# Kernel optimization log

Measured on AMD Instinct MI355X. Metric: run time of the kernel, lower is better.

The kernel has to match this reference:

```python
import jax, jax.numpy as jnp
import numpy as np
import math

B, S, D, H = 4, 2048, 1024, 16
HD = D // H  # head_dim = 64


def setup_inputs() -> dict:
    key = jax.random.key(0)
    ks = jax.random.split(key, 12)
    inv = 1.0 / math.sqrt(D)
    inp = {
        "query": jax.random.normal(ks[0], (B, S, D), dtype=jnp.float32),
        "key": jax.random.normal(ks[1], (B, S, D), dtype=jnp.float32),
        "value": jax.random.normal(ks[2], (B, S, D), dtype=jnp.float32),
        # causal mask, broadcast over heads; guarantees no all-masked softmax rows
        "mask": jnp.tril(jnp.ones((S, S), dtype=jnp.int32))[None, None].repeat(B, axis=0),
        # linear params stored as (in, out); y = x @ W + b (same math as torch Linear)
        "Wq": jax.random.uniform(ks[3], (D, D), jnp.float32, -inv, inv),
        "bq": jax.random.uniform(ks[4], (D,), jnp.float32, -inv, inv),
        "Wk": jax.random.uniform(ks[5], (D, D), jnp.float32, -inv, inv),
        "bk": jax.random.uniform(ks[6], (D,), jnp.float32, -inv, inv),
        "Wv": jax.random.uniform(ks[7], (D, D), jnp.float32, -inv, inv),
        "bv": jax.random.uniform(ks[8], (D,), jnp.float32, -inv, inv),
        "Wo": jax.random.uniform(ks[9], (D, D), jnp.float32, -inv, inv),
        "bo": jax.random.uniform(ks[10], (D,), jnp.float32, -inv, inv),
    }
    return inp


def _split_heads(x):
    # [B, S, D] -> [B, H, S, HD]
    b, s, _ = x.shape
    return x.reshape(b, s, H, HD).transpose(0, 2, 1, 3)


def reference(query, key, value, mask, Wq, bq, Wk, bk, Wv, bv, Wo, bo):
    q = _split_heads(query @ Wq + bq)   # [B,H,S,HD]
    k = _split_heads(key @ Wk + bk)
    v = _split_heads(value @ Wv + bv)
    scores = jnp.einsum("bhqd,bhkd->bhqk", q, k)          # [B,H,S,S]
    scores = jnp.where(mask == 0, -jnp.inf, scores)
    attn = jax.nn.softmax(scores / math.sqrt(HD), axis=-1)
    attn = attn * mask.astype(attn.dtype)                  # post-softmax re-mask (as in source)
    out = jnp.einsum("bhqk,bhkd->bhqd", attn, v)           # [B,H,S,HD]
    out = out.transpose(0, 2, 1, 3).reshape(query.shape[0], -1, D)
    return out @ Wo + bo
```

## Files before the change

### kernel.cpp

```cpp
#include <hip/hip_runtime.h>

typedef __attribute__((ext_vector_type(8))) short short8;
typedef __attribute__((ext_vector_type(8))) unsigned short ushort8;
typedef __attribute__((ext_vector_type(4))) unsigned short us4;
typedef __attribute__((ext_vector_type(4))) float f32x4;
typedef __attribute__((ext_vector_type(4))) int i32x4;

#define S_LEN 2048
#define D_MODEL 1024
#define N_HEADS 16
#define HEAD_DIM 64

__device__ __forceinline__ unsigned short f2bf(float f) {
  union { float f; unsigned u; } x; x.f = f;
  unsigned r = x.u + 0x7FFFu + ((x.u >> 16) & 1u);
  return (unsigned short)(r >> 16);
}

__device__ __forceinline__ int pkbf(float a, float b) {
  union { float f; unsigned u; } x, y;
  x.f = a; y.f = b;
  return (int)__builtin_amdgcn_perm(y.u + 0x8000u, x.u + 0x8000u, 0x07060302u);
}

__global__ __launch_bounds__(256) void cvt3_kernel(const float* __restrict__ a,
                                                   const float* __restrict__ b,
                                                   const float* __restrict__ c,
                                                   unsigned short* __restrict__ oa,
                                                   unsigned short* __restrict__ ob,
                                                   unsigned short* __restrict__ oc) {
  int bid = blockIdx.x;
  const float* in = (bid < 4096) ? a : (bid < 8192 ? b : c);
  unsigned short* out = (bid < 4096) ? oa : (bid < 8192 ? ob : oc);
  int i = (bid & 4095) * 256 + threadIdx.x;
  const f32x4* in4 = (const f32x4*)in;
  f32x4 x = in4[2 * i], y = in4[2 * i + 1];
  i32x4 o;
  o[0] = pkbf(x[0], x[1]);
  o[1] = pkbf(x[2], x[3]);
  o[2] = pkbf(y[0], y[1]);
  o[3] = pkbf(y[2], y[3]);
  ((i32x4*)out)[i] = o;
}

__global__ __launch_bounds__(256) void transpose_w4(
    const float* __restrict__ Wq, const float* __restrict__ Wk,
    const float* __restrict__ Wv, const float* __restrict__ Wo,
    unsigned short* __restrict__ wqkvT, unsigned short* __restrict__ woT) {
  __shared__ float tile[64][65];
  const int z = blockIdx.z;
  const float* W = (z == 0) ? Wq : (z == 1) ? Wk : (z == 2) ? Wv : Wo;
  unsigned short* Wt = (z < 3) ? (wqkvT + (size_t)z * D_MODEL * D_MODEL) : woT;
  const int no = blockIdx.x * 64, ko = blockIdx.y * 64;
  const int tx = threadIdx.x & 63, ty = threadIdx.x >> 6;
  for (int r = ty; r < 64; r += 4)
    tile[r][tx] = W[(size_t)(ko + r) * D_MODEL + no + tx];
  __syncthreads();
  for (int r = ty; r < 64; r += 4)
    Wt[(size_t)(no + r) * D_MODEL + ko + tx] = f2bf(tile[tx][r]);
}

template <int MODE>
__global__ __launch_bounds__(512) void proj_gemm(
    const unsigned short* __restrict__ A0,
    const unsigned short* __restrict__ A1,
    const unsigned short* __restrict__ A2,
    const unsigned short* __restrict__ Bt,
    const float* __restrict__ b0p, const float* __restrict__ b1p,
    const float* __restrict__ b2p,
    void* __restrict__ o0, void* __restrict__ o1, void* __restrict__ o2,
    float qscale) {
  extern __shared__ __align__(16) unsigned short smem_d[];
  const int tid = threadIdx.x;
  const int wave = tid >> 6, lane = tid & 63;
  const int quad = lane >> 4, l16 = lane & 15;

  const int nlin = blockIdx.y * (MODE == 0 ? 24 : 8) + blockIdx.x;
  const int xcd = nlin & 7;
  const int j = nlin >> 3;
  int bx_eff, by_eff;
  if (MODE == 0) {
    by_eff = xcd * 4 + ((j >> 3) & 3);
    bx_eff = (j >> 5) * 8 + (j & 7);
  } else {
    by_eff = xcd * 4 + (j >> 3);
    bx_eff = j & 7;
  }
  const int m0 = by_eff * 256, n0 = bx_eff * 128;
  const int wm = (wave >> 1) * 64, wn = (wave & 1) * 64;

  const int sel = (MODE == 0) ? (n0 >> 10) : 0;
  const unsigned short* A = (MODE == 0) ? (sel == 0 ? A0 : sel == 1 ? A1 : A2) : A0;
  const float* bias = (MODE == 0) ? (sel == 0 ? b0p : sel == 1 ? b1p : b2p) : b0p;
  const float scale = (MODE == 0 && sel == 0) ? qscale : 1.0f;
  const int nb = (MODE == 0) ? (n0 & 1023) : n0;

  f32x4 acc[4][4] = {};

  const int srw = wave * 8 + (lane >> 3);
  const int sch = ((lane & 7) ^ ((lane >> 3) & 7)) << 3;

  auto stage = [&](int kt, int half) {
    unsigned short* Ab = smem_d + (kt % 3) * 24576;
    unsigned short* Bb = Ab + 16384;
    const int k0 = kt * 64;
#pragma unroll
    for (int rr = 0; rr < 2; ++rr) {
      const int rd = half * 2 + rr;
      const unsigned short* g = A + (size_t)(m0 + rd * 64 + srw) * D_MODEL + k0 + sch;
      __builtin_amdgcn_global_load_lds((const __attribute__((address_space(1))) void*)g,
          (__attribute__((address_space(3))) void*)(Ab + rd * 4096 + wave * 512), 16, 0, 0);
    }
    const unsigned short* gb = Bt + (size_t)(n0 + half * 64 + srw) * D_MODEL + k0 + sch;
    __builtin_amdgcn_global_load_lds((const __attribute__((address_space(1))) void*)gb,
        (__attribute__((address_space(3))) void*)(Bb + half * 4096 + wave * 512), 16, 0, 0);
  };

  stage(0, 0); stage(0, 1); stage(1, 0); stage(1, 1);
  asm volatile("s_waitcnt vmcnt(6)" ::: "memory");
  __builtin_amdgcn_s_barrier();

  for (int kt = 0; kt < 16; ++kt) {
    const unsigned short* Ab = smem_d + (kt % 3) * 24576;
    const unsigned short* Bb = Ab + 16384;
#pragma unroll
    for (int t = 0; t < 2; ++t) {
      if (kt + 2 < 16) stage(kt + 2, t);
      short8 af[4], bf[4];
#pragma unroll
      for (int i = 0; i < 4; ++i) {
        int r = wm + i * 16 + l16;
        af[i] = *(const short8*)(Ab + r * 64 + (((t * 4 + quad) ^ (r & 7)) << 3));
      }
#pragma unroll
      for (int j2 = 0; j2 < 4; ++j2) {
        int r = wn + j2 * 16 + l16;
        bf[j2] = *(const short8*)(Bb + r * 64 + (((t * 4 + quad) ^ (r & 7)) << 3));
      }
      __builtin_amdgcn_s_barrier();
      __builtin_amdgcn_s_setprio(1);
#pragma unroll
      for (int i = 0; i < 4; ++i)
#pragma unroll
        for (int j2 = 0; j2 < 4; ++j2)
          acc[i][j2] = __builtin_amdgcn_mfma_f32_16x16x32_bf16(af[i], bf[j2], acc[i][j2], 0, 0, 0);
      __builtin_amdgcn_s_setprio(0);
      __builtin_amdgcn_s_barrier();
    }
    if (kt + 2 < 16) {
      asm volatile("s_waitcnt vmcnt(6)" ::: "memory");
    } else {
      asm volatile("s_waitcnt vmcnt(0)" ::: "memory");
    }
  }

  float bv4[4];
#pragma unroll
  for (int j2 = 0; j2 < 4; ++j2) bv4[j2] = bias[nb + wn + j2 * 16 + l16];

  if (MODE == 0) {
    if (sel < 2) {
      unsigned short* T = smem_d + wave * 1152;
      unsigned short* out = (unsigned short*)(sel == 0 ? o0 : o1);
      const int h = (nb + wn) >> 6;
#pragma unroll
      for (int i = 0; i < 4; ++i) {
#pragma unroll
        for (int j2 = 0; j2 < 4; ++j2)
#pragma unroll
          for (int r = 0; r < 4; ++r)
            T[(quad * 4 + r) * 72 + j2 * 16 + l16] = f2bf((acc[i][j2][r] + bv4[j2]) * scale);
        int m = m0 + wm + i * 16 + l16;
        int b = m >> 11, s = m & 2047;
#pragma unroll
        for (int t = 0; t < 2; ++t) {
          short8 row = *(const short8*)(T + l16 * 72 + t * 32 + quad * 8);
          *(short8*)(out + (((size_t)(b * N_HEADS + h) * S_LEN + s) << 6) + t * 32 + quad * 8) = row;
        }
      }
    } else {
      unsigned short* vt = (unsigned short*)o2;
#pragma unroll
      for (int i = 0; i < 4; ++i) {
        int m = m0 + wm + i * 16 + quad * 4;
        int b = m >> 11, s = m & 2047;
#pragma unroll
        for (int j2 = 0; j2 < 4; ++j2) {
          int n = nb + wn + j2 * 16 + l16;
          int h = n >> 6, d = n & 63;
          us4 pv;
#pragma unroll
          for (int r = 0; r < 4; ++r) pv[r] = f2bf(acc[i][j2][r] + bv4[j2]);
          *(us4*)(vt + (((size_t)(b * N_HEADS + h) * 64 + d) << 11) + s) = pv;
        }
      }
    }
  } else {
    float* Tf = (float*)smem_d + wave * 1088;
    float* out = (float*)o0;
#pragma unroll
    for (int i = 0; i < 4; ++i) {
#pragma unroll
      for (int j2 = 0; j2 < 4; ++j2)
#pragma unroll
        for (int r = 0; r < 4; ++r)
          Tf[(quad * 4 + r) * 68 + j2 * 16 + l16] = acc[i][j2][r] + bv4[j2];
      int m = m0 + wm + i * 16 + l16;
#pragma unroll
      for (int t = 0; t < 4; ++t) {
        f32x4 row = *(const f32x4*)(Tf + l16 * 68 + t * 16 + quad * 4);
        *(f32x4*)(out + (size_t)m * D_MODEL + nb + wn + t * 16 + quad * 4) = row;
      }
    }
  }
}

__global__ __launch_bounds__(256, 4) void flash_attn(
    const unsigned short* __restrict__ Qh,
    const unsigned short* __restrict__ Kh,
    const unsigned short* __restrict__ Vt,
    unsigned short* __restrict__ ctx) {
  __shared__ __align__(16) unsigned short smem[16384];
  const int tid = threadIdx.x;
  const int wave = tid >> 6, lane = tid & 63;
  const int quad = lane >> 4, l16 = lane & 15;
  const int l7 = l16 & 7;

  const int nlin = blockIdx.y * 16 + blockIdx.x;
  const int xcd = nlin & 7;
  const int rr = nlin >> 3;
  const int bh = xcd * 8 + (rr & 7);
  const int qslot = rr >> 3;
  const int qa = qslot & 3, qb = qslot >> 2;
  const int qbase = qa + ((qb >> 1) << 2);
  const int qi = (qb & 1) ? (15 - qbase) : qbase;
  const int q0 = qi * 128;
  const int nk = 2 * qi + 2;
  const size_t hb = (size_t)bh * (S_LEN * HEAD_DIM);
  const int srow = lane >> 3;
  const int schunk = ((lane & 7) ^ srow) * 8;

  auto stage = [&](int kt, int buf) {
    unsigned short* Kb = smem + buf * 8192;
    unsigned short* Vb = smem + buf * 8192 + 4096;
#pragma unroll
    for (int c = 0; c < 2; ++c) {
      int row = wave * 16 + c * 8 + srow;
      const unsigned short* gk = Kh + hb + (size_t)(kt * 64 + row) * 64 + schunk;
      __builtin_amdgcn_global_load_lds((const __attribute__((address_space(1))) void*)gk,
          (__attribute__((address_space(3))) void*)(Kb + (wave * 16 + c * 8) * 64), 16, 0, 0);
      const unsigned short* gv = Vt + hb + (size_t)row * S_LEN + kt * 64 + schunk;
      __builtin_amdgcn_global_load_lds((const __attribute__((address_space(1))) void*)gv,
          (__attribute__((address_space(3))) void*)(Vb + (wave * 16 + c * 8) * 64), 16, 0, 0);
    }
  };

  stage(0, 0);

  short8 qf[2][2];
#pragma unroll
  for (int s = 0; s < 2; ++s)
#pragma unroll
    for (int t = 0; t < 2; ++t)
      qf[s][t] = *(const short8*)(Qh + hb +
          (size_t)(q0 + wave * 32 + s * 16 + l16) * 64 + t * 32 + quad * 8);

  f32x4 o[4][2] = {};
  float rsum[2] = {0.f, 0.f};

  for (int kt = 0; kt < nk; ++kt) {
    __syncthreads();
    if (kt + 1 < nk) stage(kt + 1, (kt + 1) & 1);
    const unsigned short* Kb = smem + (kt & 1) * 8192;
    const unsigned short* Vb = Kb + 4096;

    if (kt * 64 > q0 + wave * 32 + 31) continue;

    f32x4 sc[2][4];
    __builtin_amdgcn_s_setprio(1);
#pragma unroll
    for (int nt = 0; nt < 4; ++nt) {
      short8 k0 = *(const short8*)(Kb + (nt * 16 + l16) * 64 + ((quad ^ l7) << 3));
      short8 k1 = *(const short8*)(Kb + (nt * 16 + l16) * 64 + (((4 + quad) ^ l7) << 3));
#pragma unroll
      for (int s = 0; s < 2; ++s) {
        f32x4 z = {};
        z = __builtin_amdgcn_mfma_f32_16x16x32_bf16(k0, qf[s][0], z, 0, 0, 0);
        sc[s][nt] = __builtin_amdgcn_mfma_f32_16x16x32_bf16(k1, qf[s][1], z, 0, 0, 0);
      }
    }
    __builtin_amdgcn_s_setprio(0);
    if (kt >= 2 * qi) {
#pragma unroll
      for (int s = 0; s < 2; ++s) {
        int qg = q0 + wave * 32 + s * 16 + l16;
#pragma unroll
        for (int nt = 0; nt < 4; ++nt) {
          int kg = kt * 64 + nt * 16 + quad * 4;
#pragma unroll
          for (int r = 0; r < 4; ++r)
            if (kg + r > qg) sc[s][nt][r] = -1e30f;
        }
      }
    }

    union { int i[4]; short8 v; } pf[2][2];
#pragma unroll
    for (int s = 0; s < 2; ++s) {
      int pk[4][2];
#pragma unroll
      for (int nt = 0; nt < 4; ++nt) {
        float p0 = __builtin_amdgcn_exp2f(sc[s][nt][0]);
        float p1 = __builtin_amdgcn_exp2f(sc[s][nt][1]);
        float p2 = __builtin_amdgcn_exp2f(sc[s][nt][2]);
        float p3 = __builtin_amdgcn_exp2f(sc[s][nt][3]);
        rsum[s] += (p0 + p1) + (p2 + p3);
        pk[nt][0] = pkbf(p0, p1);
        pk[nt][1] = pkbf(p2, p3);
      }
#pragma unroll
      for (int t = 0; t < 2; ++t) {
        int A = pk[t * 2][0], C = pk[t * 2 + 1][0];
        int B2 = pk[t * 2][1], D = pk[t * 2 + 1][1];
        asm("v_permlane32_swap_b32 %0, %1" : "+v"(A), "+v"(C));
        asm("v_permlane16_swap_b32 %0, %1" : "+v"(A), "+v"(C));
        asm("v_permlane32_swap_b32 %0, %1" : "+v"(B2), "+v"(D));
        asm("v_permlane16_swap_b32 %0, %1" : "+v"(B2), "+v"(D));
        pf[s][t].i[0] = A;
        pf[s][t].i[1] = B2;
        pf[s][t].i[2] = C;
        pf[s][t].i[3] = D;
      }
    }

    __builtin_amdgcn_s_setprio(1);
#pragma unroll
    for (int ntd = 0; ntd < 4; ++ntd) {
      short8 v0 = *(const short8*)(Vb + (ntd * 16 + l16) * 64 + ((quad ^ l7) << 3));
      short8 v1 = *(const short8*)(Vb + (ntd * 16 + l16) * 64 + (((4 + quad) ^ l7) << 3));
#pragma unroll
      for (int s = 0; s < 2; ++s) {
        o[ntd][s] = __builtin_amdgcn_mfma_f32_16x16x32_bf16(v0, pf[s][0].v, o[ntd][s], 0, 0, 0);
        o[ntd][s] = __builtin_amdgcn_mfma_f32_16x16x32_bf16(v1, pf[s][1].v, o[ntd][s], 0, 0, 0);
      }
    }
    __builtin_amdgcn_s_setprio(0);
  }

#pragma unroll
  for (int s = 0; s < 2; ++s) {
    rsum[s] += __shfl_xor(rsum[s], 16, 64);
    rsum[s] += __shfl_xor(rsum[s], 32, 64);
  }

  __syncthreads();
  unsigned short* Os = smem;
#pragma unroll
  for (int s = 0; s < 2; ++s) {
    float invl = 1.0f / rsum[s];
#pragma unroll
    for (int ntd = 0; ntd < 4; ++ntd) {
      us4 pk4;
#pragma unroll
      for (int r = 0; r < 4; ++r) pk4[r] = f2bf(o[ntd][s][r] * invl);
      *(us4*)(Os + (wave * 32 + s * 16 + l16) * 72 + ntd * 16 + quad * 4) = pk4;
    }
  }
  __syncthreads();
  const int b = bh >> 4, h = bh & 15;
#pragma unroll
  for (int it = 0; it < 4; ++it) {
    int e = it * 256 + tid;
    int row = e >> 3, c = (e & 7) * 8;
    short8 vrow = *(const short8*)(Os + row * 72 + c);
    *(short8*)(ctx + (size_t)(b * S_LEN + q0 + row) * D_MODEL + h * HEAD_DIM + c) = vrow;
  }
}

extern "C" void kernel_launch(void* const* d_in, const int* in_sizes, int n_in,
                              void* d_out, int out_size, void* d_ws, size_t ws_size,
                              hipStream_t stream) {
  (void)in_sizes; (void)n_in; (void)out_size;
  const float* q  = (const float*)d_in[0];
  const float* k  = (const float*)d_in[1];
  const float* v  = (const float*)d_in[2];
  const float* Wq = (const float*)d_in[4];
  const float* bq = (const float*)d_in[5];
  const float* Wk = (const float*)d_in[6];
  const float* bk = (const float*)d_in[7];
  const float* Wv = (const float*)d_in[8];
  const float* bv = (const float*)d_in[9];
  const float* Wo = (const float*)d_in[10];
  const float* bo = (const float*)d_in[11];
  float* out = (float*)d_out;

  if (ws_size < 109051904u) return;
  char* ws = (char*)d_ws;
  unsigned short* xq    = (unsigned short*)(ws);
  unsigned short* xk    = (unsigned short*)(ws + 16777216);
  unsigned short* xv    = (unsigned short*)(ws + 33554432);
  unsigned short* wqkvT = (unsigned short*)(ws + 50331648);
  unsigned short* woT   = (unsigned short*)(ws + 56623104);
  unsigned short* qh    = (unsigned short*)(ws + 58720256);
  unsigned short* kh    = qh + 8388608;
  unsigned short* vt    = kh + 8388608;
  unsigned short* ctx   = xq;

  static int attr_done = 0;
  if (!attr_done) {
    auto* k0f = proj_gemm<0>;
    auto* k1f = proj_gemm<1>;
    hipFuncSetAttribute(reinterpret_cast<const void*>(k0f),
                        hipFuncAttributeMaxDynamicSharedMemorySize, 147456);
    hipFuncSetAttribute(reinterpret_cast<const void*>(k1f),
                        hipFuncAttributeMaxDynamicSharedMemorySize, 147456);
    attr_done = 1;
  }

  cvt3_kernel<<<12288, 256, 0, stream>>>(q, k, v, xq, xk, xv);
  transpose_w4<<<dim3(16, 16, 4), 256, 0, stream>>>(Wq, Wk, Wv, Wo, wqkvT, woT);
  proj_gemm<0><<<dim3(24, 32), 512, 147456, stream>>>(xq, xk, xv, wqkvT, bq, bk, bv,
                                                      qh, kh, vt, 0.125f * 1.44269504088896f);
  flash_attn<<<dim3(16, 64), 256, 0, stream>>>(qh, kh, vt, ctx);
  proj_gemm<1><<<dim3(8, 32), 512, 147456, stream>>>(ctx, ctx, ctx, woT, bo, bo, bo,
                                                     out, out, out, 1.0f);
}
```

Baseline: 322.2 us.

## Shrink projection GEMM tiles to 128x128 with 256 threads and deeper K pipeline

Reworks the projection GEMM from 256x128 tiles with 512 threads and a K-step of 64 to 128x128 tiles with 256 threads, a K-step of 32 and a three-deep prefetch. LDS use drops from 144KB to 48KB, so up to three blocks can share a CU, and the grid doubles to spread work across more CUs. The block-to-XCD mapping and the LDS swizzle are remapped to match. The trade-off is less operand reuse per tile, more barriers per K iteration, and more global traffic for A and B.

```diff
diff --git a/kernel.cpp b/kernel.cpp
--- a/kernel.cpp
+++ b/kernel.cpp
@@ -61,7 +61,7 @@
 }
 
 template <int MODE>
-__global__ __launch_bounds__(512) void proj_gemm(
+__global__ __launch_bounds__(256, 3) void proj_gemm(
     const unsigned short* __restrict__ A0,
     const unsigned short* __restrict__ A1,
     const unsigned short* __restrict__ A2,
@@ -80,13 +80,15 @@
   const int j = nlin >> 3;
   int bx_eff, by_eff;
   if (MODE == 0) {
-    by_eff = xcd * 4 + ((j >> 3) & 3);
-    bx_eff = (j >> 5) * 8 + (j & 7);
+    const int sel_i = j >> 6;
+    const int rem = j & 63;
+    by_eff = xcd * 8 + (rem >> 3);
+    bx_eff = sel_i * 8 + (rem & 7);
   } else {
-    by_eff = xcd * 4 + (j >> 3);
+    by_eff = xcd * 8 + (j >> 3);
     bx_eff = j & 7;
   }
-  const int m0 = by_eff * 256, n0 = bx_eff * 128;
+  const int m0 = by_eff * 128, n0 = bx_eff * 128;
   const int wm = (wave >> 1) * 64, wn = (wave & 1) * 64;
 
   const int sel = (MODE == 0) ? (n0 >> 10) : 0;
@@ -97,61 +99,62 @@
 
   f32x4 acc[4][4] = {};
 
-  const int srw = wave * 8 + (lane >> 3);
-  const int sch = ((lane & 7) ^ ((lane >> 3) & 7)) << 3;
-
-  auto stage = [&](int kt, int half) {
-    unsigned short* Ab = smem_d + (kt % 3) * 24576;
-    unsigned short* Bb = Ab + 16384;
-    const int k0 = kt * 64;
-#pragma unroll
-    for (int rr = 0; rr < 2; ++rr) {
-      const int rd = half * 2 + rr;
-      const unsigned short* g = A + (size_t)(m0 + rd * 64 + srw) * D_MODEL + k0 + sch;
-      __builtin_amdgcn_global_load_lds((const __attribute__((address_space(1))) void*)g,
-          (__attribute__((address_space(3))) void*)(Ab + rd * 4096 + wave * 512), 16, 0, 0);
-    }
-    const unsigned short* gb = Bt + (size_t)(n0 + half * 64 + srw) * D_MODEL + k0 + sch;
-    __builtin_amdgcn_global_load_lds((const __attribute__((address_space(1))) void*)gb,
-        (__attribute__((address_space(3))) void*)(Bb + half * 4096 + wave * 512), 16, 0, 0);
+  const int lrow = lane >> 2;
+  const int kcs = ((lane & 3) ^ (lrow & 3)) << 3;
+
+  auto stage = [&](int kt) {
+    unsigned short* Ab = smem_d + (kt % 3) * 8192;
+    unsigned short* Bb = Ab + 4096;
+    const int k0 = kt * 32;
+#pragma unroll
+    for (int c = 0; c < 2; ++c) {
+      const int r = wave * 32 + c * 16;
+      const unsigned short* ga = A + (size_t)(m0 + r + lrow) * D_MODEL + k0 + kcs;
+      __builtin_amdgcn_global_load_lds((const __attribute__((address_space(1))) void*)ga,
+          (__attribute__((address_space(3))) void*)(Ab + r * 32), 16, 0, 0);
+      const unsigned short* gb = Bt + (size_t)(n0 + r + lrow) * D_MODEL + k0 + kcs;
+      __builtin_amdgcn_global_load_lds((const __attribute__((address_space(1))) void*)gb,
+          (__attribute__((address_space(3))) void*)(Bb + r * 32), 16, 0, 0);
+    }
   };
 
-  stage(0, 0); stage(0, 1); stage(1, 0); stage(1, 1);
-  asm volatile("s_waitcnt vmcnt(6)" ::: "memory");
+  const int fsw = (quad ^ (l16 & 3)) << 3;
+
+  stage(0); stage(1); stage(2);
+  asm volatile("s_waitcnt vmcnt(8)" ::: "memory");
   __builtin_amdgcn_s_barrier();
-
-  for (int kt = 0; kt < 16; ++kt) {
-    const unsigned short* Ab = smem_d + (kt % 3) * 24576;
-    const unsigned short* Bb = Ab + 16384;
-#pragma unroll
-    for (int t = 0; t < 2; ++t) {
-      if (kt + 2 < 16) stage(kt + 2, t);
-      short8 af[4], bf[4];
-#pragma unroll
-      for (int i = 0; i < 4; ++i) {
-        int r = wm + i * 16 + l16;
-        af[i] = *(const short8*)(Ab + r * 64 + (((t * 4 + quad) ^ (r & 7)) << 3));
-      }
-#pragma unroll
-      for (int j2 = 0; j2 < 4; ++j2) {
-        int r = wn + j2 * 16 + l16;
-        bf[j2] = *(const short8*)(Bb + r * 64 + (((t * 4 + quad) ^ (r & 7)) << 3));
-      }
-      __builtin_amdgcn_s_barrier();
-      __builtin_amdgcn_s_setprio(1);
-#pragma unroll
-      for (int i = 0; i < 4; ++i)
-#pragma unroll
-        for (int j2 = 0; j2 < 4; ++j2)
-          acc[i][j2] = __builtin_amdgcn_mfma_f32_16x16x32_bf16(af[i], bf[j2], acc[i][j2], 0, 0, 0);
-      __builtin_amdgcn_s_setprio(0);
-      __builtin_amdgcn_s_barrier();
-    }
-    if (kt + 2 < 16) {
-      asm volatile("s_waitcnt vmcnt(6)" ::: "memory");
-    } else {
+  __builtin_amdgcn_sched_barrier(0);
+
+  for (int kt = 0; kt < 32; ++kt) {
+    const unsigned short* Ab = smem_d + (kt % 3) * 8192;
+    const unsigned short* Bb = Ab + 4096;
+    short8 af[4], bf[4];
+#pragma unroll
+    for (int i = 0; i < 4; ++i)
+      af[i] = *(const short8*)(Ab + (wm + i * 16 + l16) * 32 + fsw);
+#pragma unroll
+    for (int i = 0; i < 4; ++i)
+      bf[i] = *(const short8*)(Bb + (wn + i * 16 + l16) * 32 + fsw);
+    asm volatile("s_waitcnt lgkmcnt(0)" ::: "memory");
+    __builtin_amdgcn_s_barrier();
+    __builtin_amdgcn_sched_barrier(0);
+    if (kt + 3 < 32) stage(kt + 3);
+    __builtin_amdgcn_s_setprio(1);
+#pragma unroll
+    for (int i = 0; i < 4; ++i)
+#pragma unroll
+      for (int j2 = 0; j2 < 4; ++j2)
+        acc[i][j2] = __builtin_amdgcn_mfma_f32_16x16x32_bf16(af[i], bf[j2], acc[i][j2], 0, 0, 0);
+    __builtin_amdgcn_s_setprio(0);
+    if (kt + 3 < 32) {
+      asm volatile("s_waitcnt vmcnt(8)" ::: "memory");
+    } else if (kt + 2 < 32) {
+      asm volatile("s_waitcnt vmcnt(4)" ::: "memory");
+    } else if (kt + 1 < 32) {
       asm volatile("s_waitcnt vmcnt(0)" ::: "memory");
     }
+    __builtin_amdgcn_s_barrier();
+    __builtin_amdgcn_sched_barrier(0);
   }
 
   float bv4[4];
@@ -411,17 +414,17 @@
     auto* k0f = proj_gemm<0>;
     auto* k1f = proj_gemm<1>;
     hipFuncSetAttribute(reinterpret_cast<const void*>(k0f),
-                        hipFuncAttributeMaxDynamicSharedMemorySize, 147456);
+                        hipFuncAttributeMaxDynamicSharedMemorySize, 49152);
     hipFuncSetAttribute(reinterpret_cast<const void*>(k1f),
-                        hipFuncAttributeMaxDynamicSharedMemorySize, 147456);
+                        hipFuncAttributeMaxDynamicSharedMemorySize, 49152);
     attr_done = 1;
   }
 
   cvt3_kernel<<<12288, 256, 0, stream>>>(q, k, v, xq, xk, xv);
   transpose_w4<<<dim3(16, 16, 4), 256, 0, stream>>>(Wq, Wk, Wv, Wo, wqkvT, woT);
-  proj_gemm<0><<<dim3(24, 32), 512, 147456, stream>>>(xq, xk, xv, wqkvT, bq, bk, bv,
-                                                      qh, kh, vt, 0.125f * 1.44269504088896f);
+  proj_gemm<0><<<dim3(24, 64), 256, 49152, stream>>>(xq, xk, xv, wqkvT, bq, bk, bv,
+                                                     qh, kh, vt, 0.125f * 1.44269504088896f);
   flash_attn<<<dim3(16, 64), 256, 0, stream>>>(qh, kh, vt, ctx);
-  proj_gemm<1><<<dim3(8, 32), 512, 147456, stream>>>(ctx, ctx, ctx, woT, bo, bo, bo,
-                                                     out, out, out, 1.0f);
-}
+  proj_gemm<1><<<dim3(8, 64), 256, 49152, stream>>>(ctx, ctx, ctx, woT, bo, bo, bo,
+                                                    out, out, out, 1.0f);
+}
```

Result: slower. 336.7 us (+4.5%).
